# Performance work log

Measured on AMD Instinct MI355X. Metric: run time of the kernel, lower is better.

Reference implementation:

```python
import jax, jax.numpy as jnp
import numpy as np

IN_FEATURES = 4096
OUT_FEATURES = 16384
I8_MAX = 127.0
I8_MIN = -128.0


def setup_inputs() -> dict:
    key = jax.random.key(0)
    kx, kw, kb = jax.random.split(key, 3)
    x = jax.random.normal(kx, (2, 4096, IN_FEATURES), dtype=jnp.float32)
    # Original nn.Linear weight [out, in]; QuantLinear stores W.T as int8 [in, out]
    w = jax.random.normal(kw, (OUT_FEATURES, IN_FEATURES), dtype=jnp.float32) * 0.02
    wt = w.T  # [in, out]
    # per-output-channel scale: max_abs over axis=0 of W.T, divided by int8 max
    weight_scale = jnp.max(jnp.abs(wt), axis=0) / I8_MAX  # [out]
    weight_q = jnp.clip(jnp.round(wt / weight_scale[None, :]), I8_MIN, I8_MAX).astype(jnp.int8)
    bias = jax.random.normal(kb, (OUT_FEATURES,), dtype=jnp.float32) * 0.02
    return {"x": x, "weight_q": weight_q, "weight_scale": weight_scale, "bias": bias}


def reference(x, weight_q, weight_scale, bias):
    # flatten leading dims -> [M, in]
    x2 = x.reshape(-1, x.shape[-1])
    # dynamic per-token activation quantization (input_scale is None in module)
    x_scale = jnp.max(jnp.abs(x2), axis=-1, keepdims=True) / I8_MAX  # [M, 1]
    x_scale = jnp.maximum(x_scale, jnp.float32(1e-12))
    x_q = jnp.clip(jnp.round(x2 / x_scale), I8_MIN, I8_MAX)  # integer-valued f32
    # scaled int8 GEMM + dequant (accumulate in f32; values exactly representable)
    acc = jnp.matmul(x_q, weight_q.astype(jnp.float32))  # [M, out]
    out = acc * x_scale * weight_scale[None, :] + bias[None, :]
    return out.reshape(*x.shape[:-1], weight_q.shape[1])
```

## Files before the change

### kernel.cpp

```cpp
#include <hip/hip_runtime.h>
#include <cstdint>
#include <cstddef>

#define IN_F  4096
#define OUT_F 16384
#define NROWS 8192
#define NKT   64

typedef __attribute__((ext_vector_type(4)))  int int32x4;
typedef __attribute__((ext_vector_type(16))) int int32x16;

__device__ __forceinline__ void gload_lds16(const void* g, void* s) {
    __builtin_amdgcn_global_load_lds((const __attribute__((address_space(1))) void*)g,
                                     (__attribute__((address_space(3))) void*)s,
                                     16, 0, 0);
}


__global__ __launch_bounds__(256) void transpose_kernel(const int* __restrict__ w,
                                                        uint8_t* __restrict__ wtS) {
    __shared__ uint8_t tile[64][68];
    const int t  = threadIdx.x;
    const int nb = blockIdx.x * 64;
    const int kt = blockIdx.y;
    const int kb = kt * 64;

#pragma unroll
    for (int p = 0; p < 4; ++p) {
        const int r = p * 16 + (t >> 4);
        const int c4 = t & 15;
        int4 u = *reinterpret_cast<const int4*>(w + (size_t)(kb + r) * OUT_F + nb + c4 * 4);
        uint32_t packed = (uint32_t)(u.x & 255) | ((uint32_t)(u.y & 255) << 8)
                        | ((uint32_t)(u.z & 255) << 16) | ((uint32_t)(u.w & 255) << 24);
        *reinterpret_cast<uint32_t*>(&tile[r][c4 * 4]) = packed;
    }
    __syncthreads();

    const int col = t >> 2;
    const int c   = t & 3;
    uint4 o;
    uint32_t* op = reinterpret_cast<uint32_t*>(&o);
#pragma unroll
    for (int j = 0; j < 4; ++j) {
        const int kk = c * 16 + j * 4;
        op[j] = (uint32_t)tile[kk][col] | ((uint32_t)tile[kk + 1][col] << 8)
              | ((uint32_t)tile[kk + 2][col] << 16) | ((uint32_t)tile[kk + 3][col] << 24);
    }
    const int ntile = nb >> 8;
    const int colg  = (nb & 255) + col;
    *reinterpret_cast<uint4*>(wtS + (((size_t)ntile * NKT + kt) * 4 + c) * 4096 + colg * 16) = o;
}

__global__ __launch_bounds__(256) void quant_kernel(const float* __restrict__ x,
                                                    uint8_t* __restrict__ xqS,
                                                    float* __restrict__ xs) {
    const int t = threadIdx.x;
    const int w = t >> 6, l = t & 63;
    const int half = l >> 5, lh = l & 31;
    const int m = blockIdx.x * 8 + w * 2 + half;
    const float* xr = x + (size_t)m * IN_F;

    float am = 0.0f;
#pragma unroll 8
    for (int jj = 0; jj < 32; ++jj) {
        float4 v = reinterpret_cast<const float4*>(xr)[jj * 32 + lh];
        am = fmaxf(am, fmaxf(fmaxf(fabsf(v.x), fabsf(v.y)),
                             fmaxf(fabsf(v.z), fabsf(v.w))));
    }
#pragma unroll
    for (int off = 16; off; off >>= 1) am = fmaxf(am, __shfl_xor(am, off));

    const float scale = fmaxf(am / 127.0f, 1e-12f);
    if (lh == 0) xs[m] = scale;

    const int mtile = m >> 8, mrow = m & 255;
    uint8_t* ob = xqS + (size_t)mtile * (NKT * 16384) + (size_t)mrow * 16;
#pragma unroll
    for (int j = 0; j < 8; ++j) {
        const int k0 = lh * 128 + j * 16;
        const float4* vp = reinterpret_cast<const float4*>(xr + k0);
        uint4 pk;
        uint32_t* pp = reinterpret_cast<uint32_t*>(&pk);
#pragma unroll
        for (int q = 0; q < 4; ++q) {
            float4 v = vp[q];
            float r0 = fminf(127.f, fmaxf(-128.f, rintf(v.x / scale)));
            float r1 = fminf(127.f, fmaxf(-128.f, rintf(v.y / scale)));
            float r2 = fminf(127.f, fmaxf(-128.f, rintf(v.z / scale)));
            float r3 = fminf(127.f, fmaxf(-128.f, rintf(v.w / scale)));
            pp[q] = ((uint32_t)((int)r0 & 255)) | ((uint32_t)((int)r1 & 255) << 8)
                  | ((uint32_t)((int)r2 & 255) << 16) | ((uint32_t)((int)r3 & 255) << 24);
        }
        const int ktk = k0 >> 6;
        const int c   = (k0 >> 4) & 3;
        *reinterpret_cast<uint4*>(ob + ((size_t)ktk * 4 + c) * 4096) = pk;
    }
}

__global__ __launch_bounds__(512, 2) void gemm_kernel(const uint8_t* __restrict__ xqS,
                                                      const uint8_t* __restrict__ wtS,
                                                      const float* __restrict__ xs,
                                                      const float* __restrict__ wsc,
                                                      const float* __restrict__ bias,
                                                      float* __restrict__ out) {
    extern __shared__ uint8_t lds[];
    uint8_t* ldsA = lds;
    uint8_t* ldsB = lds + 65536;

    const int t    = threadIdx.x;
    const int lane = t & 63;
    const int wid  = t >> 6;
    const int wm   = wid >> 2, wn = wid & 3;

    int bid = blockIdx.x;
    bid = (bid & 7) * 256 + (bid >> 3);
    const int mt = bid >> 6;
    const int nt = bid & 63;

    const uint8_t* aBase = xqS + (size_t)mt * (NKT * 16384);
    const uint8_t* bBase = wtS + (size_t)nt * (NKT * 16384);
    const int t16  = t * 16;
    const int wofs = wid * 1024;

    const int aRd0 = (lane >> 5) * 4096 + wm * 2048 + (lane & 31) * 16;
    const int bRd0 = (lane >> 5) * 4096 + wn * 1024 + (lane & 31) * 16;

    int32x16 acc[4][2] = {};

#pragma unroll
    for (int tt = 0; tt < 3; ++tt)
#pragma unroll
        for (int L = 0; L < 2; ++L) {
            gload_lds16(aBase + tt * 16384 + L * 8192 + t16, ldsA + tt * 16384 + L * 8192 + wofs);
            gload_lds16(bBase + tt * 16384 + L * 8192 + t16, ldsB + tt * 16384 + L * 8192 + wofs);
        }
    asm volatile("s_waitcnt vmcnt(8)" ::: "memory");
    __builtin_amdgcn_s_barrier();

    for (int kt = 0; kt < NKT; ++kt) {
        const int q  = (kt & 3) * 16384;
        const int q3 = ((kt + 3) & 3) * 16384;
        const size_t src3 = (size_t)(kt + 3) * 16384;

        int32x4 af[2][4], bf[2][2];
#pragma unroll
        for (int s = 0; s < 2; ++s) {
            const uint8_t* ap = ldsA + q + s * 8192 + aRd0;
            const uint8_t* bp = ldsB + q + s * 8192 + bRd0;
#pragma unroll
            for (int mr = 0; mr < 4; ++mr)
                af[s][mr] = *reinterpret_cast<const int32x4*>(ap + mr * 512);
#pragma unroll
            for (int nr = 0; nr < 2; ++nr)
                bf[s][nr] = *reinterpret_cast<const int32x4*>(bp + nr * 512);
        }

        if (kt < NKT - 3) {
#pragma unroll
            for (int L = 0; L < 2; ++L) {
                gload_lds16(aBase + src3 + L * 8192 + t16, ldsA + q3 + L * 8192 + wofs);
                gload_lds16(bBase + src3 + L * 8192 + t16, ldsB + q3 + L * 8192 + wofs);
            }
        }
        if (kt < NKT - 3)       asm volatile("s_waitcnt vmcnt(8)" ::: "memory");
        else if (kt == NKT - 3) asm volatile("s_waitcnt vmcnt(4)" ::: "memory");
        else if (kt == NKT - 2) asm volatile("s_waitcnt vmcnt(0)" ::: "memory");
        __builtin_amdgcn_s_barrier();

        __builtin_amdgcn_s_setprio(1);
#pragma unroll
        for (int s = 0; s < 2; ++s)
#pragma unroll
            for (int mr = 0; mr < 4; ++mr)
#pragma unroll
                for (int nr = 0; nr < 2; ++nr)
                    acc[mr][nr] = __builtin_amdgcn_mfma_i32_32x32x32_i8(af[s][mr], bf[s][nr], acc[mr][nr], 0, 0, 0);
        __builtin_amdgcn_s_setprio(0);
        __builtin_amdgcn_s_barrier();
    }

    const int row0 = mt * 256 + wm * 128;
    const int col0 = nt * 256 + wn * 64;
#pragma unroll
    for (int mr = 0; mr < 4; ++mr) {
        const int rbase = row0 + mr * 32 + 4 * (lane >> 5);
        float xsv[16];
#pragma unroll
        for (int g = 0; g < 16; ++g)
            xsv[g] = xs[rbase + (g & 3) + 8 * (g >> 2)];
#pragma unroll
        for (int nr = 0; nr < 2; ++nr) {
            const int n = col0 + nr * 32 + (lane & 31);
            const float ws_n = wsc[n];
            const float b_n  = bias[n];
#pragma unroll
            for (int g = 0; g < 16; ++g) {
                const int m = rbase + (g & 3) + 8 * (g >> 2);
                out[(size_t)m * OUT_F + n] = (float)acc[mr][nr][g] * xsv[g] * ws_n + b_n;
            }
        }
    }
}

extern "C" void kernel_launch(void* const* d_in, const int* in_sizes, int n_in,
                              void* d_out, int out_size, void* d_ws, size_t ws_size,
                              hipStream_t stream) {
    const float* x    = (const float*)d_in[0];
    const int*   wq   = (const int*)d_in[1];
    const float* wsc  = (const float*)d_in[2];
    const float* bias = (const float*)d_in[3];
    float* out = (float*)d_out;

    uint8_t* ws  = (uint8_t*)d_ws;
    uint8_t* wtS = ws;
    uint8_t* xqS = ws + (size_t)IN_F * OUT_F;
    float*   xs  = (float*)(ws + (size_t)IN_F * OUT_F + (size_t)NROWS * IN_F);

    (void)hipFuncSetAttribute((const void*)gemm_kernel,
                              hipFuncAttributeMaxDynamicSharedMemorySize, 131072);

    transpose_kernel<<<dim3(OUT_F / 64, IN_F / 64), 256, 0, stream>>>(wq, wtS);
    quant_kernel<<<NROWS / 8, 256, 0, stream>>>(x, xqS, xs);
    gemm_kernel<<<(NROWS / 256) * (OUT_F / 256), 512, 131072, stream>>>(xqS, wtS, xs, wsc, bias, out);
}
```

Before: 711.1 us.

## Software-pipeline LDS fragment loads across k-tiles and drop second barrier

The int8 GEMM main loop now register double-buffers the MFMA operand fragments. The first half of the next k-tile is read from LDS while the second half of the current tile is being multiplied, so LDS read latency overlaps with MFMA work. The end-of-iteration barrier is removed. The 4-stage ring stays safe because all reads of a buffer now finish (lgkmcnt(0)) before the single barrier that comes ahead of its overwrite. This adds register pressure from the extra fragment buffers and relies on sched_barrier to hold the intended instruction order.

```diff
diff --git a/kernel.cpp b/kernel.cpp
--- a/kernel.cpp
+++ b/kernel.cpp
@@ -126,6 +126,7 @@
     const int bRd0 = (lane >> 5) * 4096 + wn * 1024 + (lane & 31) * 16;
 
     int32x16 acc[4][2] = {};
+    int32x4 af0[4], bf0[2], af1[4], bf1[2];
 
 #pragma unroll
     for (int tt = 0; tt < 3; ++tt)
@@ -136,24 +137,27 @@
         }
     asm volatile("s_waitcnt vmcnt(8)" ::: "memory");
     __builtin_amdgcn_s_barrier();
+    __builtin_amdgcn_sched_barrier(0);
+
+#pragma unroll
+    for (int mr = 0; mr < 4; ++mr)
+        af0[mr] = *reinterpret_cast<const int32x4*>(ldsA + aRd0 + mr * 512);
+#pragma unroll
+    for (int nr = 0; nr < 2; ++nr)
+        bf0[nr] = *reinterpret_cast<const int32x4*>(ldsB + bRd0 + nr * 512);
 
     for (int kt = 0; kt < NKT; ++kt) {
         const int q  = (kt & 3) * 16384;
+        const int q1 = ((kt + 1) & 3) * 16384;
         const int q3 = ((kt + 3) & 3) * 16384;
         const size_t src3 = (size_t)(kt + 3) * 16384;
 
-        int32x4 af[2][4], bf[2][2];
-#pragma unroll
-        for (int s = 0; s < 2; ++s) {
-            const uint8_t* ap = ldsA + q + s * 8192 + aRd0;
-            const uint8_t* bp = ldsB + q + s * 8192 + bRd0;
-#pragma unroll
-            for (int mr = 0; mr < 4; ++mr)
-                af[s][mr] = *reinterpret_cast<const int32x4*>(ap + mr * 512);
-#pragma unroll
-            for (int nr = 0; nr < 2; ++nr)
-                bf[s][nr] = *reinterpret_cast<const int32x4*>(bp + nr * 512);
-        }
+#pragma unroll
+        for (int mr = 0; mr < 4; ++mr)
+            af1[mr] = *reinterpret_cast<const int32x4*>(ldsA + q + 8192 + aRd0 + mr * 512);
+#pragma unroll
+        for (int nr = 0; nr < 2; ++nr)
+            bf1[nr] = *reinterpret_cast<const int32x4*>(ldsB + q + 8192 + bRd0 + nr * 512);
 
         if (kt < NKT - 3) {
 #pragma unroll
@@ -162,21 +166,38 @@
                 gload_lds16(bBase + src3 + L * 8192 + t16, ldsB + q3 + L * 8192 + wofs);
             }
         }
-        if (kt < NKT - 3)       asm volatile("s_waitcnt vmcnt(8)" ::: "memory");
-        else if (kt == NKT - 3) asm volatile("s_waitcnt vmcnt(4)" ::: "memory");
-        else if (kt == NKT - 2) asm volatile("s_waitcnt vmcnt(0)" ::: "memory");
-        __builtin_amdgcn_s_barrier();
 
         __builtin_amdgcn_s_setprio(1);
 #pragma unroll
-        for (int s = 0; s < 2; ++s)
+        for (int mr = 0; mr < 4; ++mr)
+#pragma unroll
+            for (int nr = 0; nr < 2; ++nr)
+                acc[mr][nr] = __builtin_amdgcn_mfma_i32_32x32x32_i8(af0[mr], bf0[nr], acc[mr][nr], 0, 0, 0);
+        __builtin_amdgcn_s_setprio(0);
+
+        if (kt < NKT - 1) {
+            asm volatile("s_waitcnt lgkmcnt(0)" ::: "memory");
+            if (kt < NKT - 3)       asm volatile("s_waitcnt vmcnt(8)" ::: "memory");
+            else if (kt == NKT - 3) asm volatile("s_waitcnt vmcnt(4)" ::: "memory");
+            else                    asm volatile("s_waitcnt vmcnt(0)" ::: "memory");
+            __builtin_amdgcn_s_barrier();
+            __builtin_amdgcn_sched_barrier(0);
+
 #pragma unroll
             for (int mr = 0; mr < 4; ++mr)
-#pragma unroll
-                for (int nr = 0; nr < 2; ++nr)
-                    acc[mr][nr] = __builtin_amdgcn_mfma_i32_32x32x32_i8(af[s][mr], bf[s][nr], acc[mr][nr], 0, 0, 0);
+                af0[mr] = *reinterpret_cast<const int32x4*>(ldsA + q1 + aRd0 + mr * 512);
+#pragma unroll
+            for (int nr = 0; nr < 2; ++nr)
+                bf0[nr] = *reinterpret_cast<const int32x4*>(ldsB + q1 + bRd0 + nr * 512);
+        }
+
+        __builtin_amdgcn_s_setprio(1);
+#pragma unroll
+        for (int mr = 0; mr < 4; ++mr)
+#pragma unroll
+            for (int nr = 0; nr < 2; ++nr)
+                acc[mr][nr] = __builtin_amdgcn_mfma_i32_32x32x32_i8(af1[mr], bf1[nr], acc[mr][nr], 0, 0, 0);
         __builtin_amdgcn_s_setprio(0);
-        __builtin_amdgcn_s_barrier();
     }
 
     const int row0 = mt * 256 + wm * 128;
```

Result: faster. 682.2 us (-4.1%).

## Load B fragments directly from global into registers and software-pipeline A LDS reads

Applied to the files above, without the earlier changes.

The int8 weight operand is no longer staged through LDS. Each wave now loads its B fragments straight from global memory into registers, one k-tile ahead, and alternates between two register sets. Only A is staged in a 4-deep LDS ring. A fragment reads are split into two halves and interleaved with the MFMAs, so each k-step needs one barrier instead of two. LDS use drops from 128KB of dynamic memory to 64KB of static memory, which may allow two blocks per CU. The trade-off is uncoalesced 16-byte global loads for B that rely on cache reuse, and higher register pressure under the 2-block launch bound.

```diff
diff --git a/kernel.cpp b/kernel.cpp
--- a/kernel.cpp
+++ b/kernel.cpp
@@ -97,15 +97,59 @@
     }
 }
 
+#define GEMM_STEP(KT, BC, BNX)                                                        \
+    {                                                                                 \
+        const int q  = ((KT) & 3) * 16384;                                            \
+        const int q1 = (((KT) + 1) & 3) * 16384;                                      \
+        const int q3 = (((KT) + 3) & 3) * 16384;                                      \
+        if ((KT) < NKT - 1) {     \
+            const uint8_t* bsrc = bBase + (size_t)((KT) + 1) * 16384 + bOff;          \
+            BNX[0] = *reinterpret_cast<const int32x4*>(bsrc);                         \
+            BNX[1] = *reinterpret_cast<const int32x4*>(bsrc + 512);                   \
+            BNX[2] = *reinterpret_cast<const int32x4*>(bsrc + 8192);                  \
+            BNX[3] = *reinterpret_cast<const int32x4*>(bsrc + 8704);                  \
+        }                                                                             \
+        _Pragma("unroll")            \
+        for (int mr = 0; mr < 4; ++mr)                                                \
+            af1[mr] = *reinterpret_cast<const int32x4*>(ldsA + q + 8192 + aRd0 + mr * 512); \
+        if ((KT) < NKT - 3) {        \
+            _Pragma("unroll")                                                         \
+            for (int L = 0; L < 2; ++L)                                               \
+                gload_lds16(aBase + (size_t)((KT) + 3) * 16384 + L * 8192 + t16,      \
+                            ldsA + q3 + L * 8192 + wofs);                             \
+        }                                                                             \
+        __builtin_amdgcn_s_setprio(1);                                                \
+        _Pragma("unroll")                                                             \
+        for (int mr = 0; mr < 4; ++mr) {                                              \
+            acc[mr][0] = __builtin_amdgcn_mfma_i32_32x32x32_i8(af0[mr], BC[0], acc[mr][0], 0, 0, 0); \
+            acc[mr][1] = __builtin_amdgcn_mfma_i32_32x32x32_i8(af0[mr], BC[1], acc[mr][1], 0, 0, 0); \
+        }                                                                             \
+        __builtin_amdgcn_s_setprio(0);                                                \
+        if ((KT) < NKT - 1) {                                                         \
+            asm volatile("s_waitcnt lgkmcnt(0)" ::: "memory");         \
+            asm volatile("s_waitcnt vmcnt(8)" ::: "memory");    \
+            __builtin_amdgcn_s_barrier();                                             \
+            __builtin_amdgcn_sched_barrier(0);                                        \
+            _Pragma("unroll")      \
+            for (int mr = 0; mr < 4; ++mr)                                            \
+                af0[mr] = *reinterpret_cast<const int32x4*>(ldsA + q1 + aRd0 + mr * 512); \
+        }                                                                             \
+        __builtin_amdgcn_s_setprio(1);                                                \
+        _Pragma("unroll")                                                             \
+        for (int mr = 0; mr < 4; ++mr) {                                              \
+            acc[mr][0] = __builtin_amdgcn_mfma_i32_32x32x32_i8(af1[mr], BC[2], acc[mr][0], 0, 0, 0); \
+            acc[mr][1] = __builtin_amdgcn_mfma_i32_32x32x32_i8(af1[mr], BC[3], acc[mr][1], 0, 0, 0); \
+        }                                                                             \
+        __builtin_amdgcn_s_setprio(0);                                                \
+    }
+
 __global__ __launch_bounds__(512, 2) void gemm_kernel(const uint8_t* __restrict__ xqS,
                                                       const uint8_t* __restrict__ wtS,
                                                       const float* __restrict__ xs,
                                                       const float* __restrict__ wsc,
                                                       const float* __restrict__ bias,
                                                       float* __restrict__ out) {
-    extern __shared__ uint8_t lds[];
-    uint8_t* ldsA = lds;
-    uint8_t* ldsB = lds + 65536;
+    __shared__ uint8_t ldsA[65536];
 
     const int t    = threadIdx.x;
     const int lane = t & 63;
@@ -123,60 +167,33 @@
     const int wofs = wid * 1024;
 
     const int aRd0 = (lane >> 5) * 4096 + wm * 2048 + (lane & 31) * 16;
-    const int bRd0 = (lane >> 5) * 4096 + wn * 1024 + (lane & 31) * 16;
+    const int bOff = (lane >> 5) * 4096 + wn * 1024 + (lane & 31) * 16;
 
     int32x16 acc[4][2] = {};
+    int32x4 af0[4], af1[4], bfA[4], bfB[4];
 
 #pragma unroll
     for (int tt = 0; tt < 3; ++tt)
 #pragma unroll
-        for (int L = 0; L < 2; ++L) {
+        for (int L = 0; L < 2; ++L)
             gload_lds16(aBase + tt * 16384 + L * 8192 + t16, ldsA + tt * 16384 + L * 8192 + wofs);
-            gload_lds16(bBase + tt * 16384 + L * 8192 + t16, ldsB + tt * 16384 + L * 8192 + wofs);
-        }
+    {
+        const uint8_t* bsrc = bBase + bOff;
+        bfA[0] = *reinterpret_cast<const int32x4*>(bsrc);
+        bfA[1] = *reinterpret_cast<const int32x4*>(bsrc + 512);
+        bfA[2] = *reinterpret_cast<const int32x4*>(bsrc + 8192);
+        bfA[3] = *reinterpret_cast<const int32x4*>(bsrc + 8704);
+    }
     asm volatile("s_waitcnt vmcnt(8)" ::: "memory");
     __builtin_amdgcn_s_barrier();
-
-    for (int kt = 0; kt < NKT; ++kt) {
-        const int q  = (kt & 3) * 16384;
-        const int q3 = ((kt + 3) & 3) * 16384;
-        const size_t src3 = (size_t)(kt + 3) * 16384;
-
-        int32x4 af[2][4], bf[2][2];
-#pragma unroll
-        for (int s = 0; s < 2; ++s) {
-            const uint8_t* ap = ldsA + q + s * 8192 + aRd0;
-            const uint8_t* bp = ldsB + q + s * 8192 + bRd0;
-#pragma unroll
-            for (int mr = 0; mr < 4; ++mr)
-                af[s][mr] = *reinterpret_cast<const int32x4*>(ap + mr * 512);
-#pragma unroll
-            for (int nr = 0; nr < 2; ++nr)
-                bf[s][nr] = *reinterpret_cast<const int32x4*>(bp + nr * 512);
-        }
-
-        if (kt < NKT - 3) {
-#pragma unroll
-            for (int L = 0; L < 2; ++L) {
-                gload_lds16(aBase + src3 + L * 8192 + t16, ldsA + q3 + L * 8192 + wofs);
-                gload_lds16(bBase + src3 + L * 8192 + t16, ldsB + q3 + L * 8192 + wofs);
-            }
-        }
-        if (kt < NKT - 3)       asm volatile("s_waitcnt vmcnt(8)" ::: "memory");
-        else if (kt == NKT - 3) asm volatile("s_waitcnt vmcnt(4)" ::: "memory");
-        else if (kt == NKT - 2) asm volatile("s_waitcnt vmcnt(0)" ::: "memory");
-        __builtin_amdgcn_s_barrier();
-
-        __builtin_amdgcn_s_setprio(1);
-#pragma unroll
-        for (int s = 0; s < 2; ++s)
-#pragma unroll
-            for (int mr = 0; mr < 4; ++mr)
-#pragma unroll
-                for (int nr = 0; nr < 2; ++nr)
-                    acc[mr][nr] = __builtin_amdgcn_mfma_i32_32x32x32_i8(af[s][mr], bf[s][nr], acc[mr][nr], 0, 0, 0);
-        __builtin_amdgcn_s_setprio(0);
-        __builtin_amdgcn_s_barrier();
+    __builtin_amdgcn_sched_barrier(0);
+#pragma unroll
+    for (int mr = 0; mr < 4; ++mr)
+        af0[mr] = *reinterpret_cast<const int32x4*>(ldsA + aRd0 + mr * 512);
+
+    for (int kt2 = 0; kt2 < NKT; kt2 += 2) {
+        GEMM_STEP(kt2,     bfA, bfB);
+        GEMM_STEP(kt2 + 1, bfB, bfA);
     }
 
     const int row0 = mt * 256 + wm * 128;
@@ -216,10 +233,7 @@
     uint8_t* xqS = ws + (size_t)IN_F * OUT_F;
     float*   xs  = (float*)(ws + (size_t)IN_F * OUT_F + (size_t)NROWS * IN_F);
 
-    (void)hipFuncSetAttribute((const void*)gemm_kernel,
-                              hipFuncAttributeMaxDynamicSharedMemorySize, 131072);
-
     transpose_kernel<<<dim3(OUT_F / 64, IN_F / 64), 256, 0, stream>>>(wq, wtS);
     quant_kernel<<<NROWS / 8, 256, 0, stream>>>(x, xqS, xs);
-    gemm_kernel<<<(NROWS / 256) * (OUT_F / 256), 512, 131072, stream>>>(xqS, wtS, xs, wsc, bias, out);
-}
+    gemm_kernel<<<(NROWS / 256) * (OUT_F / 256), 512, 0, stream>>>(xqS, wtS, xs, wsc, bias, out);
+}
```

Result: slower. 782.2 us (+10.0%).
